# Kernel optimization log

Hardware: AMD Instinct MI355X
Metric: run time of the kernel (lower is better)

Reference implementation:

```python
import jax, jax.numpy as jnp
import numpy as np

DIM = 2048
N_HEADS = 16
HEAD_DIM = DIM // N_HEADS  # 128
KV_RANK = 512
MAX_SEQ = 2048
EPS = 1e-6


def _precompute_freqs(dim, end, theta=10000.0):
    freqs = 1.0 / theta ** (np.arange(0, dim, 2)[: dim // 2].astype(np.float32) / dim)
    t = np.arange(end, dtype=np.float32)
    ang = np.outer(t, freqs)  # [end, dim//2]
    return jnp.asarray(np.cos(ang)), jnp.asarray(np.sin(ang))


def setup_inputs() -> dict:
    key = jax.random.key(0)
    ks = jax.random.split(key, 6)
    s = 0.02
    x = jax.random.normal(ks[0], (1, 2048, DIM), dtype=jnp.float32)
    wq = jax.random.normal(ks[1], (N_HEADS * HEAD_DIM, DIM), dtype=jnp.float32) * s
    w_kv_down = jax.random.normal(ks[2], (KV_RANK, DIM), dtype=jnp.float32) * s
    w_kv_up = jax.random.normal(ks[3], (2 * N_HEADS * HEAD_DIM, KV_RANK), dtype=jnp.float32) * s
    wo = jax.random.normal(ks[4], (DIM, N_HEADS * HEAD_DIM), dtype=jnp.float32) * s
    q_norm_w = jnp.ones((HEAD_DIM,), dtype=jnp.float32)
    k_norm_w = jnp.ones((HEAD_DIM,), dtype=jnp.float32)
    freqs_cos, freqs_sin = _precompute_freqs(HEAD_DIM, MAX_SEQ)
    return {"x": x, "wq": wq, "w_kv_down": w_kv_down, "w_kv_up": w_kv_up,
            "wo": wo, "q_norm_w": q_norm_w, "k_norm_w": k_norm_w,
            "freqs_cos": freqs_cos, "freqs_sin": freqs_sin}


def _rmsnorm(x, w):
    var = jnp.mean(x * x, axis=-1, keepdims=True)
    return x * jax.lax.rsqrt(var + EPS) * w


def _rope(x, cos, sin):
    # x: [B,T,H,D] -> pairs [B,T,H,D/2,2]; cos/sin: [T,D/2] broadcast over heads
    xr = x.reshape(*x.shape[:-1], -1, 2)
    re, im = xr[..., 0], xr[..., 1]
    c = cos[None, :, None, :]
    s = sin[None, :, None, :]
    out = jnp.stack([re * c - im * s, re * s + im * c], axis=-1)
    return out.reshape(x.shape)


def reference(x, wq, w_kv_down, w_kv_up, wo, q_norm_w, k_norm_w, freqs_cos, freqs_sin):
    B, T, C = x.shape
    H, D = N_HEADS, HEAD_DIM
    xq = jnp.einsum('btc,ec->bte', x, wq).reshape(B, T, H, D)
    latent = jnp.einsum('btc,rc->btr', x, w_kv_down)            # [B,T,R]
    kv = jnp.einsum('btr,er->bte', latent, w_kv_up).reshape(B, T, 2, H, D)
    xk, xv = kv[:, :, 0], kv[:, :, 1]
    xq = _rmsnorm(xq, q_norm_w)
    xk = _rmsnorm(xk, k_norm_w)
    cos, sin = freqs_cos[:T], freqs_sin[:T]
    xq = _rope(xq, cos, sin)
    xk = _rope(xk, cos, sin)
    scale = 1.0 / jnp.sqrt(jnp.asarray(D, dtype=x.dtype))
    scores = jnp.einsum('bthd,bshd->bhts', xq, xk) * scale       # [B,H,T,T]
    causal = jnp.tril(jnp.ones((T, T), dtype=bool))
    scores = jnp.where(causal, scores, jnp.finfo(scores.dtype).min)
    attn = jax.nn.softmax(scores, axis=-1)
    out = jnp.einsum('bhts,bshd->bthd', attn, xv).reshape(B, T, C)
    return jnp.einsum('bte,ce->btc', out, wo)
```

## Files before the change

kernel.cpp:

```cpp
#include <hip/hip_runtime.h>

#define T_SEQ 2048
#define DIM   2048
#define NH    16
#define HD    128
#define KVR   512

typedef unsigned short ushort_t;
typedef __attribute__((ext_vector_type(8))) short   short8;
typedef __attribute__((ext_vector_type(8))) __bf16  bf16x8;
typedef __attribute__((ext_vector_type(4))) float   f32x4;
typedef __attribute__((ext_vector_type(4))) unsigned int u32x4;

union V8 { short8 s; bf16x8 b; u32x4 u; };

__device__ inline float b2f(ushort_t u) {
    union { unsigned u; float f; } x; x.u = ((unsigned)u) << 16; return x.f;
}
__device__ inline ushort_t f2b(float f) {
    union { float f; unsigned u; } x; x.f = f;
    unsigned r = x.u + 0x7FFFu + ((x.u >> 16) & 1u);
    return (ushort_t)(r >> 16);
}

__device__ __forceinline__ void gld16(char* lds, const ushort_t* g) {
    __builtin_amdgcn_global_load_lds(
        (const __attribute__((address_space(1))) unsigned int*)g,
        (__attribute__((address_space(3))) unsigned int*)lds,
        16, 0, 0);
}

__global__ __launch_bounds__(256) void cvtk(
    const float* __restrict__ a0, const float* __restrict__ a1,
    const float* __restrict__ a2, const float* __restrict__ a3,
    const float* __restrict__ a4,
    ushort_t* __restrict__ b0, ushort_t* __restrict__ b1,
    ushort_t* __restrict__ b2, ushort_t* __restrict__ b3,
    ushort_t* __restrict__ b4)
{
    const int N0 = 524288, N1 = 1048576, N2 = 1179648, N3 = 1441792, N4 = 1966080;
    for (int c = blockIdx.x * blockDim.x + threadIdx.x; c < N4; c += gridDim.x * blockDim.x) {
        const float* s; ushort_t* d; int off;
        if      (c < N0) { s = a0; d = b0; off = c; }
        else if (c < N1) { s = a1; d = b1; off = c - N0; }
        else if (c < N2) { s = a2; d = b2; off = c - N1; }
        else if (c < N3) { s = a3; d = b3; off = c - N2; }
        else             { s = a4; d = b4; off = c - N3; }
        f32x4 lo = *(const f32x4*)(s + (size_t)off * 8);
        f32x4 hi = *(const f32x4*)(s + (size_t)off * 8 + 4);
        V8 v;
        #pragma unroll
        for (int e = 0; e < 4; ++e) { v.b[e] = (__bf16)lo[e]; v.b[e + 4] = (__bf16)hi[e]; }
        *(u32x4*)(d + (size_t)off * 8) = v.u;
    }
}

template <bool OUT_F32>
__global__ __launch_bounds__(256) void gemm_nt(
    const ushort_t* __restrict__ A, const ushort_t* __restrict__ B,
    void* __restrict__ Cv, int M, int K,
    const ushort_t* __restrict__ B2, void* __restrict__ C2, int Nsplit, int N2)
{
    __shared__ __align__(16) char sA[2][16384];
    __shared__ __align__(16) char sB[2][16384];

    const int tid  = threadIdx.x;
    const int wave = tid >> 6;
    const int lane = tid & 63;
    const int l15  = lane & 15;
    const int l4   = lane >> 4;
    const int bm   = blockIdx.x * 128;
    const int bn   = blockIdx.y * 128;

    const ushort_t* Bp = B;
    void* Cp = Cv; int ldC = Nsplit; int bnl = bn;
    if (B2 != nullptr && bn >= Nsplit) { Bp = B2; Cp = C2; ldC = N2; bnl = bn - Nsplit; }

    const int wm = (wave >> 1) * 64;
    const int wn = (wave & 1) * 64;

    const int lp   = lane ^ ((lane >> 3) & 7);
    const int prow = lp >> 3;
    const int psub = lp & 7;
    const ushort_t* aSrc[4];
    const ushort_t* bSrc[4];
    #pragma unroll
    for (int i = 0; i < 4; ++i) {
        int r = wave * 32 + i * 8 + prow;
        aSrc[i] = A  + (size_t)(bm  + r) * K + psub * 8;
        bSrc[i] = Bp + (size_t)(bnl + r) * K + psub * 8;
    }
    const int ldsOff = wave * 4096;

    f32x4 acc[4][4] = {};
    const int nk = K >> 6;

    #pragma unroll
    for (int i = 0; i < 4; ++i) {
        gld16(&sA[0][ldsOff + i * 1024], aSrc[i]);
        gld16(&sB[0][ldsOff + i * 1024], bSrc[i]);
    }

    int cur = 0;
    for (int k = 0; k < nk; ++k) {
        __syncthreads();
        if (k + 1 < nk) {
            const int ko = (k + 1) * 64;
            #pragma unroll
            for (int i = 0; i < 4; ++i) {
                gld16(&sA[cur ^ 1][ldsOff + i * 1024], aSrc[i] + ko);
                gld16(&sB[cur ^ 1][ldsOff + i * 1024], bSrc[i] + ko);
            }
        }
        #pragma unroll
        for (int kk = 0; kk < 2; ++kk) {
            V8 a[4], b[4];
            #pragma unroll
            for (int i2 = 0; i2 < 4; ++i2) {
                int row = wm + i2 * 16 + l15;
                a[i2].u = *(const u32x4*)(sA[cur] + ((row * 128 + kk * 64 + l4 * 16) ^ ((row & 7) << 4)));
                int col = wn + i2 * 16 + l15;
                b[i2].u = *(const u32x4*)(sB[cur] + ((col * 128 + kk * 64 + l4 * 16) ^ ((col & 7) << 4)));
            }
            #pragma unroll
            for (int i2 = 0; i2 < 4; ++i2)
                #pragma unroll
                for (int j = 0; j < 4; ++j)
                    acc[i2][j] = __builtin_amdgcn_mfma_f32_16x16x32_bf16(a[i2].b, b[j].b, acc[i2][j], 0, 0, 0);
        }
        cur ^= 1;
    }

    #pragma unroll
    for (int i = 0; i < 4; ++i)
        #pragma unroll
        for (int j = 0; j < 4; ++j)
            #pragma unroll
            for (int r = 0; r < 4; ++r) {
                int rowg = bm + wm + i * 16 + l4 * 4 + r;
                int colg = bnl + wn + j * 16 + l15;
                if constexpr (OUT_F32)
                    ((float*)Cp)[(size_t)rowg * ldC + colg] = acc[i][j][r];
                else
                    ((ushort_t*)Cp)[(size_t)rowg * ldC + colg] = f2b(acc[i][j][r]);
            }
}

__global__ __launch_bounds__(256) void norm_rope2(
    ushort_t* __restrict__ Qb, ushort_t* __restrict__ KVb,
    const float* __restrict__ QW, const float* __restrict__ KW,
    const float* __restrict__ FC, const float* __restrict__ FS)
{
    const int b    = blockIdx.x;
    const bool isK = b >= 2048;
    const int t    = b & 2047;
    const int tid  = threadIdx.x;
    const int h    = tid >> 4;
    const int sub  = tid & 15;

    ushort_t* X        = isK ? KVb : Qb;
    const float* W     = isK ? KW : QW;
    const int stride   = isK ? 4096 : 2048;

    ushort_t* p = X + (size_t)t * stride + h * HD + sub * 8;
    V8 v; v.u = *(const u32x4*)p;
    float f[8];
    #pragma unroll
    for (int e = 0; e < 8; ++e) f[e] = b2f((ushort_t)v.s[e]);

    float ss = 0.f;
    #pragma unroll
    for (int e = 0; e < 8; ++e) ss += f[e] * f[e];
    ss += __shfl_xor(ss, 1);
    ss += __shfl_xor(ss, 2);
    ss += __shfl_xor(ss, 4);
    ss += __shfl_xor(ss, 8);
    float inv = rsqrtf(ss * (1.0f / 128.0f) + 1e-6f);

    float outv[8];
    #pragma unroll
    for (int k = 0; k < 4; ++k) {
        float c  = FC[(size_t)t * 64 + sub * 4 + k];
        float s  = FS[(size_t)t * 64 + sub * 4 + k];
        float w0 = W[sub * 8 + 2 * k];
        float w1 = W[sub * 8 + 2 * k + 1];
        float re = f[2 * k] * inv * w0;
        float im = f[2 * k + 1] * inv * w1;
        outv[2 * k]     = re * c - im * s;
        outv[2 * k + 1] = re * s + im * c;
    }
    V8 o;
    #pragma unroll
    for (int e = 0; e < 8; ++e) o.s[e] = (short)f2b(outv[e]);
    *(u32x4*)p = o.u;
}

#define STAGE_LOAD(kv0) do { \
  _Pragma("unroll") for (int rr = 0; rr < 4; ++rr) \
    kreg[rr] = *(const u32x4*)(KV + (size_t)((kv0) + krow[rr]) * (2 * DIM) + h * HD + kc8 * 8); \
  _Pragma("unroll") for (int rr = 0; rr < 2; ++rr) \
    _Pragma("unroll") for (int e = 0; e < 8; ++e) \
      vreg[rr][e] = *(const unsigned*)(KV + (size_t)((kv0) + vkvb[rr] * 8 + e) * (2 * DIM) + DIM + h * HD + vd); \
} while (0)

#define STAGE_WRITE(sKb, sVb) do { \
  _Pragma("unroll") for (int rr = 0; rr < 4; ++rr) \
    *(u32x4*)((sKb) + ((krow[rr] * 256 + kc8 * 16) ^ ((krow[rr] & 7) << 4))) = kreg[rr]; \
  _Pragma("unroll") for (int rr = 0; rr < 2; ++rr) { \
    V8 lo, hi; \
    _Pragma("unroll") for (int e = 0; e < 8; ++e) { \
      lo.s[e] = (short)(vreg[rr][e] & 0xFFFFu); hi.s[e] = (short)(vreg[rr][e] >> 16); } \
    *(u32x4*)((sVb) + ((vd * 128 + vkvb[rr] * 16) ^ ((vd & 7) << 4)))             = lo.u; \
    *(u32x4*)((sVb) + (((vd + 1) * 128 + vkvb[rr] * 16) ^ (((vd + 1) & 7) << 4))) = hi.u; \
  } \
} while (0)

__global__ __launch_bounds__(512) void attn_kernel(
    const ushort_t* __restrict__ Q,
    const ushort_t* __restrict__ KV,
    ushort_t* __restrict__ O)
{
    __shared__ __align__(16) char sAll[131072];

    const int id    = blockIdx.x;
    const int xcd   = id & 7;
    const int slot  = id >> 3;
    const int h     = xcd * 2 + (slot >> 4);
    const int pairb = slot & 15;

    const int tid   = threadIdx.x;
    const int gid   = tid >> 8;
    const int wtid  = tid & 255;
    const int wave4 = wtid >> 6;
    const int lane  = tid & 63;
    const int Qq    = lane & 15;
    const int G     = lane >> 4;

    char* gbase = sAll + gid * 65536;

    const int krow[4] = { (0*256 + wtid) >> 4, (1*256 + wtid) >> 4,
                          (2*256 + wtid) >> 4, (3*256 + wtid) >> 4 };
    const int kc8 = wtid & 15;
    const int vd  = lane * 2;
    const int vkvb[2] = { wave4, 4 + wave4 };

    const float scale = 0.08838834764831845f;

    u32x4 kreg[4];
    unsigned vreg[2][8];

    #pragma unroll
    for (int phase = 0; phase < 2; ++phase) {
        const int jt  = phase ? (31 - pairb) : pairb;
        const int q0w = jt * 64 + wave4 * 16;

        V8 qf[4];
        #pragma unroll
        for (int kk = 0; kk < 4; ++kk)
            qf[kk].u = *(const u32x4*)(Q + (size_t)(q0w + Qq) * DIM + h * HD + kk * 32 + G * 8);

        f32x4 o[8] = {};
        float mrow = -1e30f, lrow = 0.f;

        const int n_g = (jt >= gid) ? ((jt - gid) >> 1) + 1 : 0;
        const int nA  = (jt >> 1) + 1;

        if (n_g > 0) {
            STAGE_LOAD(gid * 64);
            STAGE_WRITE(gbase, gbase + 32768);
        }

        int cur = 0;
        for (int s = 0; s < nA; ++s) {
            __syncthreads();

            const bool pf = (s + 1 < n_g);
            if (pf) STAGE_LOAD((2 * (s + 1) + gid) * 64);

            if (s < n_g) {
                const int tcur = 2 * s + gid;
                const int kv0  = tcur * 64;
                char* sKb = gbase + cur * 16384;
                char* sVb = gbase + 32768 + cur * 16384;

                f32x4 sacc[4] = {};
                #pragma unroll
                for (int kk = 0; kk < 4; ++kk) {
                    #pragma unroll
                    for (int cb = 0; cb < 4; ++cb) {
                        int row = cb * 16 + Qq;
                        V8 kf;
                        kf.u = *(const u32x4*)(sKb + ((row * 256 + kk * 64 + G * 16) ^ ((row & 7) << 4)));
                        sacc[cb] = __builtin_amdgcn_mfma_f32_16x16x32_bf16(kf.b, qf[kk].b, sacc[cb], 0, 0, 0);
                    }
                }

                float p[4][4];
                float tmax = -3e38f;
                const int qg = q0w + Qq;
                #pragma unroll
                for (int cb = 0; cb < 4; ++cb)
                    #pragma unroll
                    for (int r = 0; r < 4; ++r) {
                        float s2 = sacc[cb][r] * scale;
                        if (tcur == jt) {
                            int kvg = kv0 + cb * 16 + G * 4 + r;
                            if (kvg > qg) s2 = -1e30f;
                        }
                        p[cb][r] = s2;
                        tmax = fmaxf(tmax, s2);
                    }
                tmax = fmaxf(tmax, __shfl_xor(tmax, 16));
                tmax = fmaxf(tmax, __shfl_xor(tmax, 32));
                float mnew = fmaxf(mrow, tmax);
                float corr = __expf(mrow - mnew);
                mrow = mnew;
                float rs = 0.f;
                #pragma unroll
                for (int cb = 0; cb < 4; ++cb)
                    #pragma unroll
                    for (int r = 0; r < 4; ++r) {
                        float e = __expf(p[cb][r] - mnew);
                        p[cb][r] = e;
                        rs += e;
                    }
                rs += __shfl_xor(rs, 16);
                rs += __shfl_xor(rs, 32);
                lrow = lrow * corr + rs;

                unsigned pk[4][2];
                #pragma unroll
                for (int cb = 0; cb < 4; ++cb) {
                    pk[cb][0] = (unsigned)f2b(p[cb][0]) | ((unsigned)f2b(p[cb][1]) << 16);
                    pk[cb][1] = (unsigned)f2b(p[cb][2]) | ((unsigned)f2b(p[cb][3]) << 16);
                }

                float cf[4];
                #pragma unroll
                for (int r = 0; r < 4; ++r)
                    cf[r] = __shfl(corr, G * 4 + r);
                #pragma unroll
                for (int nb = 0; nb < 8; ++nb)
                    #pragma unroll
                    for (int r = 0; r < 4; ++r)
                        o[nb][r] *= cf[r];

                const int sLo = ((G & 1) * 2) * 16 + Qq;
                const int sHi = sLo + 16;
                const bool hiC = (G >> 1);
                #pragma unroll
                for (int kk2 = 0; kk2 < 2; ++kk2) {
                    const int c0 = kk2 * 2, c1 = c0 + 1;
                    unsigned w0a = __shfl(pk[c0][0], sLo), w0b = __shfl(pk[c1][0], sLo);
                    unsigned w1a = __shfl(pk[c0][1], sLo), w1b = __shfl(pk[c1][1], sLo);
                    unsigned w2a = __shfl(pk[c0][0], sHi), w2b = __shfl(pk[c1][0], sHi);
                    unsigned w3a = __shfl(pk[c0][1], sHi), w3b = __shfl(pk[c1][1], sHi);
                    V8 pa;
                    pa.u[0] = hiC ? w0b : w0a;
                    pa.u[1] = hiC ? w1b : w1a;
                    pa.u[2] = hiC ? w2b : w2a;
                    pa.u[3] = hiC ? w3b : w3a;
                    #pragma unroll
                    for (int nb = 0; nb < 8; ++nb) {
                        int d = nb * 16 + Qq;
                        V8 vf;
                        vf.u = *(const u32x4*)(sVb + ((d * 128 + kk2 * 64 + G * 16) ^ ((d & 7) << 4)));
                        o[nb] = __builtin_amdgcn_mfma_f32_16x16x32_bf16(pa.b, vf.b, o[nb], 0, 0, 0);
                    }
                }
            }

            if (pf) STAGE_WRITE(gbase + (cur ^ 1) * 16384, gbase + 32768 + (cur ^ 1) * 16384);
            cur ^= 1;
        }

        __syncthreads();
        float* mrg = (float*)sAll;
        float* mlb = (float*)(sAll + 33792);
        if (gid == 1) {
            #pragma unroll
            for (int nb = 0; nb < 8; ++nb)
                #pragma unroll
                for (int r = 0; r < 4; ++r) {
                    int qloc = wave4 * 16 + G * 4 + r;
                    mrg[qloc * 132 + nb * 16 + Qq] = o[nb][r];
                }
            if (G == 0) {
                int qloc = wave4 * 16 + Qq;
                mlb[qloc]      = mrow;
                mlb[64 + qloc] = lrow;
            }
        }
        __syncthreads();
        if (gid == 0) {
            int qloc0 = wave4 * 16 + Qq;
            float mB = mlb[qloc0], lB = mlb[64 + qloc0];
            float m  = fmaxf(mrow, mB);
            float cA = __expf(mrow - m), cB = __expf(mB - m);
            float linv = 1.f / (lrow * cA + lB * cB);
            float cAr[4], cBr[4], lir[4];
            #pragma unroll
            for (int r = 0; r < 4; ++r) {
                cAr[r] = __shfl(cA, G * 4 + r);
                cBr[r] = __shfl(cB, G * 4 + r);
                lir[r] = __shfl(linv, G * 4 + r);
            }
            #pragma unroll
            for (int nb = 0; nb < 8; ++nb)
                #pragma unroll
                for (int r = 0; r < 4; ++r) {
                    int qloc = wave4 * 16 + G * 4 + r;
                    float ob  = mrg[qloc * 132 + nb * 16 + Qq];
                    float val = (o[nb][r] * cAr[r] + ob * cBr[r]) * lir[r];
                    int qgr = jt * 64 + qloc;
                    O[(size_t)qgr * DIM + h * HD + nb * 16 + Qq] = f2b(val);
                }
        }
        __syncthreads();
    }
}

extern "C" void kernel_launch(void* const* d_in, const int* in_sizes, int n_in,
                              void* d_out, int out_size, void* d_ws, size_t ws_size,
                              hipStream_t stream)
{
    const float* x    = (const float*)d_in[0];
    const float* wq   = (const float*)d_in[1];
    const float* wkvd = (const float*)d_in[2];
    const float* wkvu = (const float*)d_in[3];
    const float* wo   = (const float*)d_in[4];
    const float* qnw  = (const float*)d_in[5];
    const float* knw  = (const float*)d_in[6];
    const float* fc   = (const float*)d_in[7];
    const float* fs   = (const float*)d_in[8];
    float* out = (float*)d_out;

    char* ws = (char*)d_ws;
    const size_t MB = 1024 * 1024;
    ushort_t* xb    = (ushort_t*)(ws);
    ushort_t* att   = (ushort_t*)(ws);
    ushort_t* Qb    = (ushort_t*)(ws + 8  * MB);
    ushort_t* wqb   = (ushort_t*)(ws + 16 * MB);
    ushort_t* wkvdb = (ushort_t*)(ws + 24 * MB);
    ushort_t* kvb   = (ushort_t*)(ws + 16 * MB);
    ushort_t* lat   = (ushort_t*)(ws + 32 * MB);
    ushort_t* wkvub = (ushort_t*)(ws + 34 * MB);
    ushort_t* wob   = (ushort_t*)(ws + 38 * MB);

    cvtk<<<dim3(2048), dim3(256), 0, stream>>>(x, wq, wkvd, wkvu, wo,
                                               xb, wqb, wkvdb, wkvub, wob);
    gemm_nt<false><<<dim3(16, 20), dim3(256), 0, stream>>>(xb, wqb, Qb, 2048, 2048,
                                                           wkvdb, lat, 2048, 512);
    gemm_nt<false><<<dim3(16, 32), dim3(256), 0, stream>>>(lat, wkvub, kvb, 2048, 512,
                                                           nullptr, nullptr, 4096, 0);
    norm_rope2<<<dim3(4096), dim3(256), 0, stream>>>(Qb, kvb, qnw, knw, fc, fs);
    attn_kernel<<<dim3(256), dim3(512), 0, stream>>>(Qb, kvb, att);
    gemm_nt<true><<<dim3(16, 16), dim3(256), 0, stream>>>(att, wob, out, 2048, 2048,
                                                          nullptr, nullptr, 2048, 0);
}
```

Before: 171.2 us.

## Add lazy softmax rescale, exp2 domain, MFMA priority, GEMM block swizzle

Moves the attention softmax into the exp2 domain by folding log2(e) into the score scale. It skips the running-max update and the output rescale when no lane's max grows beyond a threshold, which removes the per-tile correction multiply in the common case. It also raises wave priority around the MFMA loops and remaps GEMM block indices with an XCD-style swizzle, plus an occupancy hint of 2 blocks per SM. The lazy rescale lets exponentials grow up to 2^THR relative to the stored max. That is numerically safe in fp32, but the probabilities are packed to bf16 values that can exceed 1.

```diff
diff --git a/kernel.cpp b/kernel.cpp
--- a/kernel.cpp
+++ b/kernel.cpp
@@ -56,7 +56,7 @@
 }
 
 template <bool OUT_F32>
-__global__ __launch_bounds__(256) void gemm_nt(
+__global__ __launch_bounds__(256, 2) void gemm_nt(
     const ushort_t* __restrict__ A, const ushort_t* __restrict__ B,
     void* __restrict__ Cv, int M, int K,
     const ushort_t* __restrict__ B2, void* __restrict__ C2, int Nsplit, int N2)
@@ -69,8 +69,13 @@
     const int lane = tid & 63;
     const int l15  = lane & 15;
     const int l4   = lane >> 4;
-    const int bm   = blockIdx.x * 128;
-    const int bn   = blockIdx.y * 128;
+
+    const int gridX = gridDim.x;
+    int idlin = blockIdx.y * gridX + blockIdx.x;
+    const int cpx = (gridX * gridDim.y) >> 3;
+    idlin = (idlin & 7) * cpx + (idlin >> 3);
+    const int bm = (idlin % gridX) * 128;
+    const int bn = (idlin / gridX) * 128;
 
     const ushort_t* Bp = B;
     void* Cp = Cv; int ldC = Nsplit; int bnl = bn;
@@ -158,9 +163,9 @@
     const int h    = tid >> 4;
     const int sub  = tid & 15;
 
-    ushort_t* X        = isK ? KVb : Qb;
-    const float* W     = isK ? KW : QW;
-    const int stride   = isK ? 4096 : 2048;
+    ushort_t* X      = isK ? KVb : Qb;
+    const float* W   = isK ? KW : QW;
+    const int stride = isK ? 4096 : 2048;
 
     ushort_t* p = X + (size_t)t * stride + h * HD + sub * 8;
     V8 v; v.u = *(const u32x4*)p;
@@ -244,7 +249,8 @@
     const int vd  = lane * 2;
     const int vkvb[2] = { wave4, 4 + wave4 };
 
-    const float scale = 0.08838834764831845f;
+    const float scale2 = 0.08838834764831845f * 1.4426950408889634f;
+    const float THR2   = 11.541560327111707f;
 
     u32x4 kreg[4];
     unsigned vreg[2][8];
@@ -284,6 +290,7 @@
                 char* sVb = gbase + 32768 + cur * 16384;
 
                 f32x4 sacc[4] = {};
+                __builtin_amdgcn_s_setprio(1);
                 #pragma unroll
                 for (int kk = 0; kk < 4; ++kk) {
                     #pragma unroll
@@ -294,6 +301,7 @@
                         sacc[cb] = __builtin_amdgcn_mfma_f32_16x16x32_bf16(kf.b, qf[kk].b, sacc[cb], 0, 0, 0);
                     }
                 }
+                __builtin_amdgcn_s_setprio(0);
 
                 float p[4][4];
                 float tmax = -3e38f;
@@ -302,7 +310,7 @@
                 for (int cb = 0; cb < 4; ++cb)
                     #pragma unroll
                     for (int r = 0; r < 4; ++r) {
-                        float s2 = sacc[cb][r] * scale;
+                        float s2 = sacc[cb][r] * scale2;
                         if (tcur == jt) {
                             int kvg = kv0 + cb * 16 + G * 4 + r;
                             if (kvg > qg) s2 = -1e30f;
@@ -312,15 +320,20 @@
                     }
                 tmax = fmaxf(tmax, __shfl_xor(tmax, 16));
                 tmax = fmaxf(tmax, __shfl_xor(tmax, 32));
-                float mnew = fmaxf(mrow, tmax);
-                float corr = __expf(mrow - mnew);
-                mrow = mnew;
+
+                const bool skip = __all(tmax - mrow <= THR2);
+                float corr = 1.0f;
+                if (!skip) {
+                    const float mnew = fmaxf(mrow, tmax);
+                    corr = exp2f(mrow - mnew);
+                    mrow = mnew;
+                }
                 float rs = 0.f;
                 #pragma unroll
                 for (int cb = 0; cb < 4; ++cb)
                     #pragma unroll
                     for (int r = 0; r < 4; ++r) {
-                        float e = __expf(p[cb][r] - mnew);
+                        float e = exp2f(p[cb][r] - mrow);
                         p[cb][r] = e;
                         rs += e;
                     }
@@ -335,15 +348,17 @@
                     pk[cb][1] = (unsigned)f2b(p[cb][2]) | ((unsigned)f2b(p[cb][3]) << 16);
                 }
 
-                float cf[4];
-                #pragma unroll
-                for (int r = 0; r < 4; ++r)
-                    cf[r] = __shfl(corr, G * 4 + r);
-                #pragma unroll
-                for (int nb = 0; nb < 8; ++nb)
+                if (!skip) {
+                    float cf[4];
                     #pragma unroll
                     for (int r = 0; r < 4; ++r)
-                        o[nb][r] *= cf[r];
+                        cf[r] = __shfl(corr, G * 4 + r);
+                    #pragma unroll
+                    for (int nb = 0; nb < 8; ++nb)
+                        #pragma unroll
+                        for (int r = 0; r < 4; ++r)
+                            o[nb][r] *= cf[r];
+                }
 
                 const int sLo = ((G & 1) * 2) * 16 + Qq;
                 const int sHi = sLo + 16;
@@ -360,6 +375,7 @@
                     pa.u[1] = hiC ? w1b : w1a;
                     pa.u[2] = hiC ? w2b : w2a;
                     pa.u[3] = hiC ? w3b : w3a;
+                    __builtin_amdgcn_s_setprio(1);
                     #pragma unroll
                     for (int nb = 0; nb < 8; ++nb) {
                         int d = nb * 16 + Qq;
@@ -367,6 +383,7 @@
                         vf.u = *(const u32x4*)(sVb + ((d * 128 + kk2 * 64 + G * 16) ^ ((d & 7) << 4)));
                         o[nb] = __builtin_amdgcn_mfma_f32_16x16x32_bf16(pa.b, vf.b, o[nb], 0, 0, 0);
                     }
+                    __builtin_amdgcn_s_setprio(0);
                 }
             }
 
@@ -396,7 +413,7 @@
             int qloc0 = wave4 * 16 + Qq;
             float mB = mlb[qloc0], lB = mlb[64 + qloc0];
             float m  = fmaxf(mrow, mB);
-            float cA = __expf(mrow - m), cB = __expf(mB - m);
+            float cA = exp2f(mrow - m), cB = exp2f(mB - m);
             float linv = 1.f / (lrow * cA + lB * cB);
             float cAr[4], cBr[4], lir[4];
             #pragma unroll
```

After: 174.3 us. Within noise of the previous version (+1.8%).
